# Performance work log

Hardware: AMD Instinct MI355X
Metric: run time of the kernel (lower is better)

The kernel has to match this reference:

```python
import jax, jax.numpy as jnp
import numpy as np

H = 128
W = 128
DELTA = 7000.0  # sigmainv in the original (delta default 7000)


def setup_inputs() -> dict:
    key = jax.random.key(0)
    k1, k2, k3, k4 = jax.random.split(key, 4)
    B, P, F, TH, TW = 2, 300, 512, 512, 512
    points_bxpx3 = jax.random.uniform(k1, (B, P, 3), jnp.float32) * 2.0 - 1.0  # NDC cube [-1,1]
    faces_fx3 = jax.random.randint(k2, (F, 3), 0, P, dtype=jnp.int32)
    uv_bxpx2 = jax.random.uniform(k3, (B, P, 2), jnp.float32)  # texcoords in [0,1]
    texture_bx3xthxtw = jax.random.uniform(k4, (B, 3, TH, TW), jnp.float32)
    return {"points_bxpx3": points_bxpx3, "faces_fx3": faces_fx3,
            "uv_bxpx2": uv_bxpx2, "texture_bx3xthxtw": texture_bx3xthxtw}


def _edge(ax, ay, bx, by, px, py):
    # signed area * 2 of triangle (a, b, p); standard edge function
    return (bx - ax) * (py - ay) - (by - ay) * (px - ax)


def _seg_d2(ax, ay, bx, by, px, py):
    # squared distance from point p to segment (a, b)
    abx, aby = bx - ax, by - ay
    apx, apy = px - ax, py - ay
    denom = abx * abx + aby * aby + 1e-12
    t = jnp.clip((apx * abx + apy * aby) / denom, 0.0, 1.0)
    dx = apx - t * abx
    dy = apy - t * aby
    return dx * dx + dy * dy


def _rasterize(points_bxpx3, faces_fx3, feats_bxfx3xd, height, width, delta):
    """Soft DIB-R-style rasterizer.
    Returns (imfeat [B,H,W,D], improb [B,H,W,1]).
    """
    B = points_bxpx3.shape[0]
    v = points_bxpx3[:, faces_fx3]                      # (B,F,3,3) gathered face vertices
    x0, x1, x2 = (v[:, :, i, 0][:, :, None, None] for i in range(3))
    y0, y1, y2 = (v[:, :, i, 1][:, :, None, None] for i in range(3))
    z0, z1, z2 = (v[:, :, i, 2][:, :, None, None] for i in range(3))

    # pixel-center grid in NDC; y flipped (top row = +1)
    px = ((jnp.arange(width, dtype=points_bxpx3.dtype) + 0.5) / width * 2.0 - 1.0)[None, None, None, :]
    py = (1.0 - (jnp.arange(height, dtype=points_bxpx3.dtype) + 0.5) / height * 2.0)[None, None, :, None]

    area = _edge(x0, y0, x1, y1, x2, y2)                # (B,F,1,1) == normal_z (cross-product z)
    front = area > 1e-8                                  # front-facing (normalz > 0) cull
    inv_area = 1.0 / jnp.where(front, area, 1.0)

    w0 = _edge(x1, y1, x2, y2, px, py) * inv_area        # (B,F,H,W) barycentrics
    w1 = _edge(x2, y2, x0, y0, px, py) * inv_area
    w2 = _edge(x0, y0, x1, y1, px, py) * inv_area
    inside = front & (w0 >= 0) & (w1 >= 0) & (w2 >= 0)

    z_pix = w0 * z0 + w1 * z1 + w2 * z2                  # interpolated depth
    zbuf = jnp.where(inside, z_pix, -1e9)
    best = jnp.argmax(zbuf, axis=1)                      # (B,H,W) nearest covering face
    hit = jnp.any(inside, axis=1)[..., None].astype(points_bxpx3.dtype)  # (B,H,W,1)

    # gather winning barycentrics and per-face vertex features
    w = jnp.stack([w0, w1, w2], axis=-1)                 # (B,F,H,W,3)
    idx = jnp.broadcast_to(best[:, None, :, :, None], (B, 1, height, width, 3))
    wb = jnp.take_along_axis(w, idx, axis=1)[:, 0]       # (B,H,W,3)
    fb = jax.vmap(lambda f, i: f[i])(feats_bxfx3xd, best)  # (B,H,W,3,D)
    imfeat = jnp.einsum('bhwk,bhwkd->bhwd', wb, fb) * hit

    # soft coverage: prob of each face = exp(-delta * d2(pixel, triangle)); z-buffer blend
    d2 = jnp.minimum(
        jnp.minimum(_seg_d2(x0, y0, x1, y1, px, py), _seg_d2(x1, y1, x2, y2, px, py)),
        _seg_d2(x2, y2, x0, y0, px, py))
    d2 = jnp.where(inside, 0.0, d2)
    p = jnp.where(front, jnp.exp(-delta * d2), 0.0)      # (B,F,H,W)
    log_miss = jnp.sum(jnp.log1p(-jnp.clip(p, 0.0, 1.0 - 1e-7)), axis=1)  # (B,H,W)
    improb = (1.0 - jnp.exp(log_miss))[..., None]
    return imfeat, improb


def _fragmentshader(imtexcoords, texture_bx3xthxtw, hardmask):
    # bilinear texture sampling; background is zero
    B, C, TH, TW = texture_bx3xthxtw.shape
    u = jnp.clip(imtexcoords[..., 0], 0.0, 1.0)
    vv = jnp.clip(imtexcoords[..., 1], 0.0, 1.0)
    fx = u * (TW - 1)
    fy = (1.0 - vv) * (TH - 1)
    x0 = jnp.floor(fx).astype(jnp.int32); x1 = jnp.minimum(x0 + 1, TW - 1)
    y0 = jnp.floor(fy).astype(jnp.int32); y1 = jnp.minimum(y0 + 1, TH - 1)
    wx = (fx - x0)[:, None]; wy = (fy - y0)[:, None]     # (B,1,H,W)

    def g(tex, yy, xx):  # tex (C,TH,TW), yy/xx (H,W) -> (C,H,W)
        return tex[:, yy, xx]
    c00 = jax.vmap(g)(texture_bx3xthxtw, y0, x0)
    c01 = jax.vmap(g)(texture_bx3xthxtw, y0, x1)
    c10 = jax.vmap(g)(texture_bx3xthxtw, y1, x0)
    c11 = jax.vmap(g)(texture_bx3xthxtw, y1, x1)
    col = (c00 * (1 - wx) * (1 - wy) + c01 * wx * (1 - wy)
           + c10 * (1 - wx) * wy + c11 * wx * wy)        # (B,C,H,W)
    return col.transpose(0, 2, 3, 1) * hardmask          # (B,H,W,C)


def reference(points_bxpx3, faces_fx3, uv_bxpx2, texture_bx3xthxtw):
    # texture mode: per-face vertex features = [u, v, mask=1]
    uvf = uv_bxpx2[:, faces_fx3]                          # (B,F,3,2)
    ones = jnp.ones_like(uvf[..., :1])
    feats = jnp.concatenate([uvf, ones], axis=-1)         # (B,F,3,3)
    imfeat, improb = _rasterize(points_bxpx3, faces_fx3, feats, H, W, DELTA)
    imtexcoords = imfeat[..., :2]
    hardmask = jax.lax.stop_gradient(imfeat[..., 2:3])    # .detach() in the original
    imrender = _fragmentshader(imtexcoords, texture_bx3xthxtw, hardmask)
    return imrender, improb
```

## Files before the change

kernel.cpp:

```cpp
#include <hip/hip_runtime.h>
#include <math.h>

constexpr int kB = 2, kP = 300, kF = 512, kH = 128, kW = 128, kTH = 512, kTW = 512;
constexpr float kDelta = 7000.0f;
constexpr float kCut = 0.06f;
constexpr float kThr = 0.1374f;
constexpr float kLogInside = -15.9423847f;

__global__ __launch_bounds__(512, 6) void render_all(const float* __restrict__ pts,
                                                     const int* __restrict__ faces,
                                                     const float* __restrict__ uvs,
                                                     const float* __restrict__ tex,
                                                     float* __restrict__ out) {
    __shared__ float4 s_hot4[kF * 3];
    __shared__ float2 s_vtx[kF * 3];
    __shared__ unsigned short s_of[kF];
    __shared__ int s_wsum[8];
    __shared__ float s_bz[512];
    __shared__ int s_bi[512];
    __shared__ float s_lm[512];

    int tile = (int)blockIdx.x;
    int b = tile >> 8;
    int rem = tile & 255;
    int ty = rem >> 4, tx = rem & 15;
    int tid = (int)threadIdx.x;
    int lane = tid & 63;
    int wv = tid >> 6;

    {
        int f = tid;
        int i0 = faces[f * 3 + 0], i1 = faces[f * 3 + 1], i2 = faces[f * 3 + 2];
        const float* pb = pts + b * kP * 3;
        float x0 = pb[i0 * 3], y0 = pb[i0 * 3 + 1], z0 = pb[i0 * 3 + 2];
        float x1 = pb[i1 * 3], y1 = pb[i1 * 3 + 1], z1 = pb[i1 * 3 + 2];
        float x2 = pb[i2 * 3], y2 = pb[i2 * 3 + 1], z2 = pb[i2 * 3 + 2];
        float area = (x1 - x0) * (y2 - y0) - (y1 - y0) * (x2 - x0);
        bool front = area > 1e-8f;

        s_hot4[f * 3 + 0] = make_float4(0.0f, 0.0f, -1e30f, 0.0f);
        unsigned long long bal = __ballot(front);
        if (lane == 0) s_wsum[wv] = __popcll(bal);
        __syncthreads();

        int base = 0;
#pragma unroll
        for (int w = 0; w < 8; ++w) base += (w < wv) ? s_wsum[w] : 0;
        int slot = base + __popcll(bal & ((1ull << lane) - 1ull));

        if (front) {
            float inv_a = 1.0f / area;
            float e0x = x2 - x1, e0y = y2 - y1;
            float e1x = x0 - x2, e1y = y0 - y2;
            float e2x = x1 - x0, e2y = y1 - y0;
            float l0 = fmaf(e0x, e0x, e0y * e0y);
            float l1 = fmaf(e1x, e1x, e1y * e1y);
            float l2 = fmaf(e2x, e2x, e2y * e2y);
            float s0 = rsqrtf(l0 + 1e-12f);
            float s1 = rsqrtf(l1 + 1e-12f);
            float s2 = rsqrtf(l2 + 1e-12f);
            float A0 = -e0y * s0, B0 = e0x * s0, C0 = (e0y * x1 - e0x * y1) * s0;
            float A1 = -e1y * s1, B1 = e1x * s1, C1 = (e1y * x2 - e1x * y2) * s1;
            float A2 = -e2y * s2, B2 = e2x * s2, C2 = (e2y * x0 - e2x * y0) * s2;
            float a0 = -e0y * inv_a, b0 = e0x * inv_a, c0 = (e0y * x1 - e0x * y1) * inv_a;
            float a1 = -e1y * inv_a, b1 = e1x * inv_a, c1 = (e1y * x2 - e1x * y2) * inv_a;
            float a2 = -e2y * inv_a, b2 = e2x * inv_a, c2 = (e2y * x0 - e2x * y0) * inv_a;
            s_hot4[slot * 3 + 0] = make_float4(A0, B0, C0, A1);
            s_hot4[slot * 3 + 1] = make_float4(B1, C1, A2, B2);
            s_hot4[slot * 3 + 2] = make_float4(C2,
                                               a0 * z0 + a1 * z1 + a2 * z2,
                                               b0 * z0 + b1 * z1 + b2 * z2,
                                               c0 * z0 + c1 * z1 + c2 * z2);
            s_vtx[slot * 3 + 0] = make_float2(x0, y0);
            s_vtx[slot * 3 + 1] = make_float2(x1, y1);
            s_vtx[slot * 3 + 2] = make_float2(x2, y2);
            s_of[slot] = (unsigned short)f;
        }
    }
    __syncthreads();

    int pyi = ty * 8 + (lane >> 3);
    int pxi = tx * 8 + (lane & 7);
    float px = ((float)pxi + 0.5f) * (2.0f / 128.0f) - 1.0f;
    float py = 1.0f - ((float)pyi + 0.5f) * (2.0f / 128.0f);

    float cx = (float)(tx * 8 + 4) * (2.0f / 128.0f) - 1.0f;
    float cy = 1.0f - (float)(ty * 8 + 4) * (2.0f / 128.0f);
    int slt = (wv << 6) + lane;
    float4 g0 = s_hot4[slt * 3 + 0];
    float4 g1 = s_hot4[slt * 3 + 1];
    float4 g2 = s_hot4[slt * 3 + 2];
    float Lc0 = fmaf(g0.x, cx, fmaf(g0.y, cy, g0.z));
    float Lc1 = fmaf(g0.w, cx, fmaf(g1.x, cy, g1.y));
    float Lc2 = fmaf(g1.z, cx, fmaf(g1.w, cy, g2.x));
    float minc = fminf(fminf(Lc0, Lc1), Lc2);
    unsigned long long m = __ballot(minc >= -kThr);

    float bestz = -1e9f;
    int besti = -1, icnt = 0;
    float lm = 0.0f;

    while (m) {
        int l = (int)__builtin_ctzll(m);
        m &= (m - 1);
        int fs = (wv << 6) + l;
        float4 h0 = s_hot4[fs * 3 + 0];
        float4 h1 = s_hot4[fs * 3 + 1];
        float4 h2 = s_hot4[fs * 3 + 2];
        float L0 = fmaf(h0.x, px, fmaf(h0.y, py, h0.z));
        float L1 = fmaf(h0.w, px, fmaf(h1.x, py, h1.y));
        float L2 = fmaf(h1.z, px, fmaf(h1.w, py, h2.x));
        float minL = fminf(fminf(L0, L1), L2);
        bool inside = minL >= 0.0f;
        float z = fmaf(h2.y, px, fmaf(h2.z, py, h2.w));
        if (inside && z > bestz) { bestz = z; besti = fs; }
        icnt += inside ? 1 : 0;
        float db = fminf(fminf(fabsf(L0), fabsf(L1)), fabsf(L2));
        bool need = (!inside) & (db < kCut);
        if (__any(need)) {
            float2 v0 = s_vtx[fs * 3 + 0];
            float2 v1 = s_vtx[fs * 3 + 1];
            float2 v2 = s_vtx[fs * 3 + 2];
            float e0x = v2.x - v1.x, e0y = v2.y - v1.y;
            float e1x = v0.x - v2.x, e1y = v0.y - v2.y;
            float e2x = v1.x - v0.x, e2y = v1.y - v0.y;
            float p0x = px - v0.x, p0y = py - v0.y;
            float p1x = px - v1.x, p1y = py - v1.y;
            float p2x = px - v2.x, p2y = py - v2.y;
            float dot0 = fmaf(p1x, e0x, p1y * e0y), len0 = fmaf(e0x, e0x, e0y * e0y);
            float dot1 = fmaf(p2x, e1x, p2y * e1y), len1 = fmaf(e1x, e1x, e1y * e1y);
            float dot2 = fmaf(p0x, e2x, p0y * e2y), len2 = fmaf(e2x, e2x, e2y * e2y);
            float c0 = (dot0 >= 0.0f && dot0 <= len0) ? L0 * L0 : 1e30f;
            float c1 = (dot1 >= 0.0f && dot1 <= len1) ? L1 * L1 : 1e30f;
            float c2 = (dot2 >= 0.0f && dot2 <= len2) ? L2 * L2 : 1e30f;
            float dv0 = fmaf(p0x, p0x, p0y * p0y);
            float dv1 = fmaf(p1x, p1x, p1y * p1y);
            float dv2 = fmaf(p2x, p2x, p2y * p2y);
            float d2 = fminf(fminf(fminf(c0, c1), fminf(c2, dv0)), fminf(dv1, dv2));
            float p = __expf(-kDelta * d2);
            p = fminf(p, 1.0f - 1e-7f);
            float lp = __logf(1.0f - p);
            lm += need ? lp : 0.0f;
        }
    }
    lm = fmaf((float)icnt, kLogInside, lm);

    s_bz[tid] = bestz;
    s_bi[tid] = besti;
    s_lm[tid] = lm;
    __syncthreads();

    if (tid < 64) {
        float bz = s_bz[tid];
        int bi = s_bi[tid];
        float L = s_lm[tid];
#pragma unroll
        for (int w = 1; w < 8; ++w) {
            float z2 = s_bz[w * 64 + tid];
            int ii = s_bi[w * 64 + tid];
            L += s_lm[w * 64 + tid];
            if (z2 > bz || (z2 == bz && ii >= 0 && (unsigned)ii < (unsigned)bi)) {
                bz = z2; bi = ii;
            }
        }
        float improb = 1.0f - expf(L);
        float u = 0.0f, v = 0.0f, mk = 0.0f;
        if (bi >= 0) {
            float2 v0 = s_vtx[bi * 3 + 0];
            float2 v1 = s_vtx[bi * 3 + 1];
            float2 v2 = s_vtx[bi * 3 + 2];
            float area = (v1.x - v0.x) * (v2.y - v0.y) - (v1.y - v0.y) * (v2.x - v0.x);
            float inv_a = 1.0f / area;
            float w0 = ((v2.x - v1.x) * (py - v1.y) - (v2.y - v1.y) * (px - v1.x)) * inv_a;
            float w1 = ((v0.x - v2.x) * (py - v2.y) - (v0.y - v2.y) * (px - v2.x)) * inv_a;
            float w2 = ((v1.x - v0.x) * (py - v0.y) - (v1.y - v0.y) * (px - v0.x)) * inv_a;
            int of = (int)s_of[bi];
            int j0 = faces[of * 3], j1 = faces[of * 3 + 1], j2 = faces[of * 3 + 2];
            const float* ub = uvs + b * kP * 2;
            u = w0 * ub[j0 * 2] + w1 * ub[j1 * 2] + w2 * ub[j2 * 2];
            v = w0 * ub[j0 * 2 + 1] + w1 * ub[j1 * 2 + 1] + w2 * ub[j2 * 2 + 1];
            mk = w0 + w1 + w2;
        }
        float uc = fminf(fmaxf(u, 0.0f), 1.0f);
        float vc = fminf(fmaxf(v, 0.0f), 1.0f);
        float fx = uc * (float)(kTW - 1);
        float fy = (1.0f - vc) * (float)(kTH - 1);
        int xi0 = (int)floorf(fx), yi0 = (int)floorf(fy);
        int xi1 = min(xi0 + 1, kTW - 1), yi1 = min(yi0 + 1, kTH - 1);
        float wx = fx - (float)xi0, wy = fy - (float)yi0;
        float w00 = (1.0f - wx) * (1.0f - wy);
        float w01 = wx * (1.0f - wy);
        float w10 = (1.0f - wx) * wy;
        float w11 = wx * wy;
        int o00 = yi0 * kTW + xi0, o01 = yi0 * kTW + xi1;
        int o10 = yi1 * kTW + xi0, o11 = yi1 * kTW + xi1;
        const float* tb = tex + (size_t)b * 3 * kTH * kTW;
        float cols[3];
#pragma unroll
        for (int c = 0; c < 3; ++c) {
            const float* tc = tb + c * kTH * kTW;
            cols[c] = (tc[o00] * w00 + tc[o01] * w01 + tc[o10] * w10 + tc[o11] * w11) * mk;
        }
        int pix = (b * kH + pyi) * kW + pxi;
        out[pix * 3 + 0] = cols[0];
        out[pix * 3 + 1] = cols[1];
        out[pix * 3 + 2] = cols[2];
        out[kB * kH * kW * 3 + pix] = improb;
    }
}

extern "C" void kernel_launch(void* const* d_in, const int* in_sizes, int n_in,
                              void* d_out, int out_size, void* d_ws, size_t ws_size,
                              hipStream_t stream) {
    const float* pts = (const float*)d_in[0];
    const int* faces = (const int*)d_in[1];
    const float* uvs = (const float*)d_in[2];
    const float* tex = (const float*)d_in[3];
    float* out = (float*)d_out;
    render_all<<<kB * 256, 512, 0, stream>>>(pts, faces, uvs, tex, out);
}
```

Baseline: 20.38 us.

## Tighten tile face culling with exact segment distance and interleave face slots

The per-tile face admission test changes from a signed-edge-distance threshold to a true squared point-to-triangle distance from the tile centre, admitting fewer faces per tile. Compacted faces are now spread round-robin across the eight waves so each wave's ballot loop gets a balanced share, and the interleaved index keeps the original face order for depth tie-breaking. Face data moves from one interleaved float4 array into three separate arrays, and empty slots get sentinel vertices. This adds a per-thread distance computation up front in exchange for fewer and more even loop iterations per wave.

```diff
diff --git a/kernel.cpp b/kernel.cpp
--- a/kernel.cpp
+++ b/kernel.cpp
@@ -4,7 +4,7 @@
 constexpr int kB = 2, kP = 300, kF = 512, kH = 128, kW = 128, kTH = 512, kTW = 512;
 constexpr float kDelta = 7000.0f;
 constexpr float kCut = 0.06f;
-constexpr float kThr = 0.1374f;
+constexpr float kThr2 = 0.018882f;
 constexpr float kLogInside = -15.9423847f;
 
 __global__ __launch_bounds__(512, 6) void render_all(const float* __restrict__ pts,
@@ -12,7 +12,7 @@
                                                      const float* __restrict__ uvs,
                                                      const float* __restrict__ tex,
                                                      float* __restrict__ out) {
-    __shared__ float4 s_hot4[kF * 3];
+    __shared__ float4 sA[kF], sB[kF], sC[kF];
     __shared__ float2 s_vtx[kF * 3];
     __shared__ unsigned short s_of[kF];
     __shared__ int s_wsum[8];
@@ -38,7 +38,12 @@
         float area = (x1 - x0) * (y2 - y0) - (y1 - y0) * (x2 - x0);
         bool front = area > 1e-8f;
 
-        s_hot4[f * 3 + 0] = make_float4(0.0f, 0.0f, -1e30f, 0.0f);
+        sA[f] = make_float4(0.0f, 0.0f, -1e30f, 0.0f);
+        sB[f] = make_float4(0.0f, -1e30f, 0.0f, 0.0f);
+        sC[f] = make_float4(-1e30f, 0.0f, 0.0f, 0.0f);
+        s_vtx[f * 3 + 0] = make_float2(1e15f, 1e15f);
+        s_vtx[f * 3 + 1] = make_float2(1e15f, 1e15f);
+        s_vtx[f * 3 + 2] = make_float2(1e15f, 1e15f);
         unsigned long long bal = __ballot(front);
         if (lane == 0) s_wsum[wv] = __popcll(bal);
         __syncthreads();
@@ -46,9 +51,10 @@
         int base = 0;
 #pragma unroll
         for (int w = 0; w < 8; ++w) base += (w < wv) ? s_wsum[w] : 0;
-        int slot = base + __popcll(bal & ((1ull << lane) - 1ull));
+        int k = base + __popcll(bal & ((1ull << lane) - 1ull));
 
         if (front) {
+            int slot = ((k & 7) << 6) | (k >> 3);
             float inv_a = 1.0f / area;
             float e0x = x2 - x1, e0y = y2 - y1;
             float e1x = x0 - x2, e1y = y0 - y2;
@@ -65,12 +71,12 @@
             float a0 = -e0y * inv_a, b0 = e0x * inv_a, c0 = (e0y * x1 - e0x * y1) * inv_a;
             float a1 = -e1y * inv_a, b1 = e1x * inv_a, c1 = (e1y * x2 - e1x * y2) * inv_a;
             float a2 = -e2y * inv_a, b2 = e2x * inv_a, c2 = (e2y * x0 - e2x * y0) * inv_a;
-            s_hot4[slot * 3 + 0] = make_float4(A0, B0, C0, A1);
-            s_hot4[slot * 3 + 1] = make_float4(B1, C1, A2, B2);
-            s_hot4[slot * 3 + 2] = make_float4(C2,
-                                               a0 * z0 + a1 * z1 + a2 * z2,
-                                               b0 * z0 + b1 * z1 + b2 * z2,
-                                               c0 * z0 + c1 * z1 + c2 * z2);
+            sA[slot] = make_float4(A0, B0, C0, A1);
+            sB[slot] = make_float4(B1, C1, A2, B2);
+            sC[slot] = make_float4(C2,
+                                   a0 * z0 + a1 * z1 + a2 * z2,
+                                   b0 * z0 + b1 * z1 + b2 * z2,
+                                   c0 * z0 + c1 * z1 + c2 * z2);
             s_vtx[slot * 3 + 0] = make_float2(x0, y0);
             s_vtx[slot * 3 + 1] = make_float2(x1, y1);
             s_vtx[slot * 3 + 2] = make_float2(x2, y2);
@@ -86,15 +92,38 @@
 
     float cx = (float)(tx * 8 + 4) * (2.0f / 128.0f) - 1.0f;
     float cy = 1.0f - (float)(ty * 8 + 4) * (2.0f / 128.0f);
-    int slt = (wv << 6) + lane;
-    float4 g0 = s_hot4[slt * 3 + 0];
-    float4 g1 = s_hot4[slt * 3 + 1];
-    float4 g2 = s_hot4[slt * 3 + 2];
-    float Lc0 = fmaf(g0.x, cx, fmaf(g0.y, cy, g0.z));
-    float Lc1 = fmaf(g0.w, cx, fmaf(g1.x, cy, g1.y));
-    float Lc2 = fmaf(g1.z, cx, fmaf(g1.w, cy, g2.x));
-    float minc = fminf(fminf(Lc0, Lc1), Lc2);
-    unsigned long long m = __ballot(minc >= -kThr);
+    unsigned long long m;
+    {
+        int slt = (wv << 6) + lane;
+        float4 a4 = sA[slt];
+        float4 b4 = sB[slt];
+        float4 c4 = sC[slt];
+        float L0 = fmaf(a4.x, cx, fmaf(a4.y, cy, a4.z));
+        float L1 = fmaf(a4.w, cx, fmaf(b4.x, cy, b4.y));
+        float L2 = fmaf(b4.z, cx, fmaf(b4.w, cy, c4.x));
+        float minc = fminf(fminf(L0, L1), L2);
+        float2 v0 = s_vtx[slt * 3 + 0];
+        float2 v1 = s_vtx[slt * 3 + 1];
+        float2 v2 = s_vtx[slt * 3 + 2];
+        float e0x = v2.x - v1.x, e0y = v2.y - v1.y;
+        float e1x = v0.x - v2.x, e1y = v0.y - v2.y;
+        float e2x = v1.x - v0.x, e2y = v1.y - v0.y;
+        float p0x = cx - v0.x, p0y = cy - v0.y;
+        float p1x = cx - v1.x, p1y = cy - v1.y;
+        float p2x = cx - v2.x, p2y = cy - v2.y;
+        float dot0 = fmaf(p1x, e0x, p1y * e0y), len0 = fmaf(e0x, e0x, e0y * e0y);
+        float dot1 = fmaf(p2x, e1x, p2y * e1y), len1 = fmaf(e1x, e1x, e1y * e1y);
+        float dot2 = fmaf(p0x, e2x, p0y * e2y), len2 = fmaf(e2x, e2x, e2y * e2y);
+        float c0 = (dot0 >= 0.0f && dot0 <= len0) ? L0 * L0 : 1e30f;
+        float c1 = (dot1 >= 0.0f && dot1 <= len1) ? L1 * L1 : 1e30f;
+        float c2 = (dot2 >= 0.0f && dot2 <= len2) ? L2 * L2 : 1e30f;
+        float dv0 = fmaf(p0x, p0x, p0y * p0y);
+        float dv1 = fmaf(p1x, p1x, p1y * p1y);
+        float dv2 = fmaf(p2x, p2x, p2y * p2y);
+        float d2c = fminf(fminf(fminf(c0, c1), fminf(c2, dv0)), fminf(dv1, dv2));
+        bool admit = (minc >= 0.0f) | (d2c <= kThr2);
+        m = __ballot(admit);
+    }
 
     float bestz = -1e9f;
     int besti = -1, icnt = 0;
@@ -104,16 +133,17 @@
         int l = (int)__builtin_ctzll(m);
         m &= (m - 1);
         int fs = (wv << 6) + l;
-        float4 h0 = s_hot4[fs * 3 + 0];
-        float4 h1 = s_hot4[fs * 3 + 1];
-        float4 h2 = s_hot4[fs * 3 + 2];
+        int k = (l << 3) | wv;
+        float4 h0 = sA[fs];
+        float4 h1 = sB[fs];
+        float4 h2 = sC[fs];
         float L0 = fmaf(h0.x, px, fmaf(h0.y, py, h0.z));
         float L1 = fmaf(h0.w, px, fmaf(h1.x, py, h1.y));
         float L2 = fmaf(h1.z, px, fmaf(h1.w, py, h2.x));
         float minL = fminf(fminf(L0, L1), L2);
         bool inside = minL >= 0.0f;
         float z = fmaf(h2.y, px, fmaf(h2.z, py, h2.w));
-        if (inside && z > bestz) { bestz = z; besti = fs; }
+        if (inside && z > bestz) { bestz = z; besti = k; }
         icnt += inside ? 1 : 0;
         float db = fminf(fminf(fabsf(L0), fabsf(L1)), fabsf(L2));
         bool need = (!inside) & (db < kCut);
@@ -166,15 +196,16 @@
         float improb = 1.0f - expf(L);
         float u = 0.0f, v = 0.0f, mk = 0.0f;
         if (bi >= 0) {
-            float2 v0 = s_vtx[bi * 3 + 0];
-            float2 v1 = s_vtx[bi * 3 + 1];
-            float2 v2 = s_vtx[bi * 3 + 2];
+            int slot = ((bi & 7) << 6) | (bi >> 3);
+            float2 v0 = s_vtx[slot * 3 + 0];
+            float2 v1 = s_vtx[slot * 3 + 1];
+            float2 v2 = s_vtx[slot * 3 + 2];
             float area = (v1.x - v0.x) * (v2.y - v0.y) - (v1.y - v0.y) * (v2.x - v0.x);
             float inv_a = 1.0f / area;
             float w0 = ((v2.x - v1.x) * (py - v1.y) - (v2.y - v1.y) * (px - v1.x)) * inv_a;
             float w1 = ((v0.x - v2.x) * (py - v2.y) - (v0.y - v2.y) * (px - v2.x)) * inv_a;
             float w2 = ((v1.x - v0.x) * (py - v0.y) - (v1.y - v0.y) * (px - v0.x)) * inv_a;
-            int of = (int)s_of[bi];
+            int of = (int)s_of[slot];
             int j0 = faces[of * 3], j1 = faces[of * 3 + 1], j2 = faces[of * 3 + 2];
             const float* ub = uvs + b * kP * 2;
             u = w0 * ub[j0 * 2] + w1 * ub[j1 * 2] + w2 * ub[j2 * 2];
```

Measured after the change: 18.32 us. -10.1%, faster.
